# Performance work log

Measured on AMD Instinct MI355X. Metric: run time of the kernel, lower is better.

The kernel has to match this reference:

```python
import jax, jax.numpy as jnp
import numpy as np

B, LQ, LKV = 2, 4096, 2048
DQ = DK = DV = 1024
H, DQK, DHV = 16, 64, 64
DOUT = 1024


def _band_mask(span, stride):
    # additive mask: 0 where 0 <= row - col*stride < span, else -inf
    rows = jnp.arange(LQ)[:, None]
    cols = jnp.arange(LKV)[None, :]
    s = rows - cols * stride
    valid = (s >= 0) & (s < span)
    return jnp.where(valid, 0.0, -jnp.inf).astype(jnp.float32)  # [LQ, LKV]


def setup_inputs() -> dict:
    key = jax.random.key(0)
    ks = jax.random.split(key, 7)
    return {
        "q": jax.random.normal(ks[0], (B, LQ, DQ), jnp.float32),
        "k": jax.random.normal(ks[1], (B, LKV, DK), jnp.float32),
        "v": jax.random.normal(ks[2], (B, LKV, DV), jnp.float32),
        # Linear weights stored as [in, out] (x @ W == torch Linear with W.T)
        "Wq": jax.random.normal(ks[3], (DQ, H * DQK), jnp.float32) / np.sqrt(DQ).astype(np.float32),
        "Wk": jax.random.normal(ks[4], (DK, H * DQK), jnp.float32) / np.sqrt(DK).astype(np.float32),
        "Wv": jax.random.normal(ks[5], (DV, H * DHV), jnp.float32) / np.sqrt(DV).astype(np.float32),
        "Wo": jax.random.normal(ks[6], (H * DHV, DOUT), jnp.float32) / np.sqrt(H * DHV).astype(np.float32),
        "span": 16,
        "stride": 2,
    }


def reference(q, k, v, Wq, Wk, Wv, Wo, span, stride):
    mask = _band_mask(span, stride)  # [LQ, LKV]
    Q = (q @ Wq).reshape(B, LQ, H, DQK)   # [B, LQ, H, DQK]
    K = (k @ Wk).reshape(B, LKV, H, DQK)  # [B, LKV, H, DQK]
    V = (v @ Wv).reshape(B, LKV, H, DHV)  # [B, LKV, H, DHV]
    scores = jnp.einsum("bqhd,bkhd->bhqk", Q, K) + mask  # [B, H, LQ, LKV]
    # NOTE: original code softmaxes over dim 2 == the QUERY axis (faithful)
    attn = jax.nn.softmax(scores, axis=2)
    ctx = jnp.einsum("bhqk,bkhd->bqhd", attn, V).reshape(B, LQ, H * DHV)
    return ctx @ Wo  # [B, LQ, DOUT]
```

## Files before the change

### kernel.cpp

```cpp
#include <hip/hip_runtime.h>
#include <cstdint>
#include <cstddef>


typedef _Float16 f16;
typedef _Float16 f16x4 __attribute__((ext_vector_type(4)));
typedef _Float16 f16x8 __attribute__((ext_vector_type(8)));
typedef float v4f __attribute__((ext_vector_type(4)));

#define B_  2
#define LQ_ 4096
#define LKV_ 2048
#define DMODEL 1024
#define NH 16
#define HD 64
#define SPAN 16
#define STRIDE 2

#define NQ_ELEMS  ((size_t)B_ * LQ_ * DMODEL)
#define NKV_ELEMS ((size_t)B_ * LKV_ * DMODEL)

__device__ __forceinline__ void async_copy16(const f16* g, f16* l) {
    __builtin_amdgcn_global_load_lds((const __attribute__((address_space(1))) void*)g,
                                     (__attribute__((address_space(3))) void*)l, 16, 0, 0);
}

__global__ __launch_bounds__(256)
void transpose_all(const float* __restrict__ W0, const float* __restrict__ W1,
                   const float* __restrict__ W2, const float* __restrict__ W3,
                   f16* __restrict__ T0, f16* __restrict__ T1,
                   f16* __restrict__ T2, f16* __restrict__ T3) {
    const int t = threadIdx.x;
    const int bid = blockIdx.x;
    const int z = bid >> 8, rem = bid & 255;
    const int bx = rem & 15, byy = rem >> 4;
    const float* W;
    f16* Wt;
    switch (z) {
        case 0: W = W0; Wt = T0; break;
        case 1: W = W1; Wt = T1; break;
        case 2: W = W2; Wt = T2; break;
        default: W = W3; Wt = T3; break;
    }
    __shared__ float tile[64][65];
    const int r0 = byy * 64, c0 = bx * 64;
    const int tx = t & 63, ty = t >> 6;
    for (int i = ty; i < 64; i += 4)
        tile[i][tx] = W[(long)(r0 + i) * DMODEL + c0 + tx];
    __syncthreads();
    for (int i = ty; i < 64; i += 4)
        Wt[(long)(c0 + i) * DMODEL + r0 + tx] = (f16)tile[tx][i];
}

template <bool OUT_F32, bool A_F32>
__device__ __forceinline__ void gemm_body(const void* __restrict__ Av,
                                          const f16* __restrict__ Bt,
                                          void* __restrict__ Cv,
                                          int rowTile, int colTile) {
    constexpr int K = DMODEL, N = DMODEL;
    __shared__ f16 As[128 * 64];
    __shared__ f16 Bs[128 * 64];
    const int t = threadIdx.x;
    const int lane = t & 63;
    const int w = t >> 6;
    const int wm = w >> 1, wn = w & 1;
    const long rowBase = (long)rowTile * 128;
    const long colBase = (long)colTile * 128;
    const int qrow = lane & 15;
    const int quad = lane >> 4;

    v4f acc[4][4] = {};

    const int srow = t >> 3;
    const int schunk = t & 7;
    const int gchunk = schunk ^ (srow & 7);
    const f16* aptrH = (const f16*)Av + (rowBase + srow) * (long)K + gchunk * 8;
    const float* aptrF = (const float*)Av + (rowBase + srow) * (long)K + gchunk * 8;
    const f16* bptr = Bt + (colBase + srow) * (long)K + gchunk * 8;
    f16* lA = &As[srow * 64 + schunk * 8];
    f16* lB = &Bs[srow * 64 + schunk * 8];

    for (int k0 = 0; k0 < K; k0 += 64) {
#pragma unroll
        for (int i = 0; i < 4; ++i)
            async_copy16(bptr + k0 + i * 32 * (long)K, lB + i * 2048);
        if (A_F32) {
            float4 lo[4], hi[4];
#pragma unroll
            for (int i = 0; i < 4; ++i) {
                lo[i] = *(const float4*)(aptrF + k0 + i * 32 * (long)K);
                hi[i] = *(const float4*)(aptrF + k0 + i * 32 * (long)K + 4);
            }
#pragma unroll
            for (int i = 0; i < 4; ++i) {
                f16x8 o = {(f16)lo[i].x, (f16)lo[i].y, (f16)lo[i].z, (f16)lo[i].w,
                           (f16)hi[i].x, (f16)hi[i].y, (f16)hi[i].z, (f16)hi[i].w};
                *(f16x8*)(lA + i * 2048) = o;
            }
        } else {
#pragma unroll
            for (int i = 0; i < 4; ++i)
                async_copy16(aptrH + k0 + i * 32 * (long)K, lA + i * 2048);
        }
        __syncthreads();
#pragma unroll
        for (int s = 0; s < 2; ++s) {
            const int xk = (s * 4 + quad) ^ (qrow & 7);
            f16x8 af[4], bf[4];
#pragma unroll
            for (int mt = 0; mt < 4; ++mt)
                af[mt] = *(const f16x8*)(&As[(wm * 64 + mt * 16 + qrow) * 64 + xk * 8]);
#pragma unroll
            for (int nt = 0; nt < 4; ++nt)
                bf[nt] = *(const f16x8*)(&Bs[(wn * 64 + nt * 16 + qrow) * 64 + xk * 8]);
#pragma unroll
            for (int mt = 0; mt < 4; ++mt)
#pragma unroll
                for (int nt = 0; nt < 4; ++nt)
                    acc[mt][nt] = __builtin_amdgcn_mfma_f32_16x16x32_f16(
                        af[mt], bf[nt], acc[mt][nt], 0, 0, 0);
        }
        __syncthreads();
    }

#pragma unroll
    for (int mt = 0; mt < 4; ++mt)
#pragma unroll
        for (int nt = 0; nt < 4; ++nt) {
            const long col = colBase + wn * 64 + nt * 16 + qrow;
#pragma unroll
            for (int r = 0; r < 4; ++r) {
                const long row = rowBase + wm * 64 + mt * 16 + quad * 4 + r;
                if (OUT_F32)
                    ((float*)Cv)[row * (long)N + col] = acc[mt][nt][r];
                else
                    ((f16*)Cv)[row * (long)N + col] = (f16)acc[mt][nt][r];
            }
        }
}

__global__ __launch_bounds__(256, 2)
void gemm_qkv(const float* __restrict__ A0, const float* __restrict__ A1,
              const float* __restrict__ A2, const f16* __restrict__ B0,
              const f16* __restrict__ B1, const f16* __restrict__ B2,
              f16* __restrict__ C0, f16* __restrict__ C1, f16* __restrict__ C2) {
    const int id = blockIdx.x;
    const int xcd = id & 7;
    const int g = id >> 3;
    const int ct = g & 7;
    int rowIdx = (g >> 3) + xcd * 16;
    const float* A;
    const f16* Bt;
    f16* C;
    if (rowIdx < 64) {
        A = A0; Bt = B0; C = C0;
    } else if (rowIdx < 96) {
        A = A1; Bt = B1; C = C1; rowIdx -= 64;
    } else {
        A = A2; Bt = B2; C = C2; rowIdx -= 96;
    }
    gemm_body<false, true>((const void*)A, Bt, (void*)C, rowIdx, ct);
}

__global__ __launch_bounds__(256, 2)
void gemm_out(const f16* __restrict__ A, const f16* __restrict__ Bt,
              float* __restrict__ C) {
    const int id = blockIdx.x;
    const int xcd = id & 7;
    const int g = id >> 3;
    const int ct = g & 7;
    const int rowIdx = (g >> 3) + xcd * 8;
    gemm_body<true, false>((const void*)A, Bt, (void*)C, rowIdx, ct);
}

__global__ __launch_bounds__(256)
void attn_scores(const f16* __restrict__ Q, const f16* __restrict__ Km,
                 float* __restrict__ attnw) {
    const int c0 = blockIdx.x * 4, b = blockIdx.y;
    const int t = threadIdx.x;
    __shared__ f16 Qs[24 * 1032];
    __shared__ f16 Ks[4 * 1032];

#pragma unroll
    for (int it = 0; it < 12; ++it) {
        const int ch = t + 256 * it;
        const int row = ch >> 7, off = (ch & 127) * 8;
        int qq = 2 * c0 + row;
        if (qq > LQ_ - 1) qq = LQ_ - 1;
        f16x8 x = *(const f16x8*)(Q + (size_t)(b * LQ_ + qq) * DMODEL + off);
        const int h = off >> 6, bb = (off >> 3) & 7;
        *(f16x8*)(&Qs[row * 1032 + h * 64 + ((bb + h) & 7) * 8]) = x;
    }
#pragma unroll
    for (int it = 0; it < 2; ++it) {
        const int ch = t + 256 * it;
        const int row = ch >> 7, off = (ch & 127) * 8;
        f16x8 x = *(const f16x8*)(Km + (size_t)(b * LKV_ + c0 + row) * DMODEL + off);
        const int h = off >> 6, bb = (off >> 3) & 7;
        *(f16x8*)(&Ks[row * 1032 + h * 64 + ((bb + h) & 7) * 8]) = x;
    }
    __syncthreads();

    const int h = t >> 4, j = t & 15;
#pragma unroll
    for (int ci = 0; ci < 4; ++ci) {
        const int c = c0 + ci;
        const int q = STRIDE * c + j;
        const int row = 2 * ci + j;
        float a = 0.f;
#pragma unroll
        for (int bb = 0; bb < 8; ++bb) {
            const int off = h * 64 + ((bb + h) & 7) * 8;
            f16x8 qv = *(const f16x8*)(&Qs[row * 1032 + off]);
            f16x8 kv = *(const f16x8*)(&Ks[ci * 1032 + off]);
#pragma unroll
            for (int u = 0; u < 8; ++u) a += (float)qv[u] * (float)kv[u];
        }
        float s = (q < LQ_) ? a : -1e30f;
        float m = s;
#pragma unroll
        for (int o = 1; o < 16; o <<= 1) m = fmaxf(m, __shfl_xor(m, o, 64));
        float p = (q < LQ_) ? __expf(s - m) : 0.f;
        float sum = p;
#pragma unroll
        for (int o = 1; o < 16; o <<= 1) sum += __shfl_xor(sum, o, 64);
        attnw[(size_t)((b * LKV_ + c) * NH + h) * SPAN + j] = p / sum;
    }
}

__global__ __launch_bounds__(256)
void ctx_gather(const float* __restrict__ attnw, const f16* __restrict__ V,
                f16* __restrict__ ctx) {
    const int q0 = blockIdx.x * 16, b = blockIdx.y;
    const int t = threadIdx.x;
    const int kbase = (q0 >> 1) - 7;
    __shared__ f16 Vs[16 * 1024];
    __shared__ float A_lds[16 * 256];

#pragma unroll
    for (int it = 0; it < 8; ++it) {
        const int ch = t + 256 * it;
        const int row = ch >> 7, off = (ch & 127) * 8;
        int k = kbase + row;
        k = (k < 0) ? 0 : ((k > LKV_ - 1) ? LKV_ - 1 : k);
        *(f16x8*)(&Vs[row * 1024 + off]) =
            *(const f16x8*)(V + (size_t)(b * LKV_ + k) * DMODEL + off);
    }
#pragma unroll
    for (int it = 0; it < 4; ++it) {
        const int ch = t + 256 * it;
        const int row = ch >> 6, off = (ch & 63) * 4;
        int k = kbase + row;
        k = (k < 0) ? 0 : ((k > LKV_ - 1) ? LKV_ - 1 : k);
        *(float4*)(&A_lds[row * 256 + off]) =
            *(const float4*)(attnw + (size_t)(b * LKV_ + k) * 256 + off);
    }
    __syncthreads();

    const int d = t & 63;
    const int hg = t >> 6;
#pragma unroll
    for (int ql = 0; ql < 16; ++ql) {
        const int q = q0 + ql;
        const int j0 = q & 1;
        float acc[4] = {0.f, 0.f, 0.f, 0.f};
#pragma unroll
        for (int i = 0; i < SPAN / STRIDE; ++i) {
            const int kq = (q >> 1) - i;
            if (kq < 0) break;
            const int rr = kq - kbase;
#pragma unroll
            for (int hh = 0; hh < 4; ++hh) {
                const int h = hg * 4 + hh;
                acc[hh] += A_lds[rr * 256 + h * 16 + j0 + 2 * i] *
                           (float)Vs[rr * 1024 + h * 64 + d];
            }
        }
        f16* crow = ctx + (size_t)(b * LQ_ + q) * DMODEL;
#pragma unroll
        for (int hh = 0; hh < 4; ++hh) {
            const int h = hg * 4 + hh;
            crow[h * HD + d] = (f16)acc[hh];
        }
    }
}

extern "C" void kernel_launch(void* const* d_in, const int* in_sizes, int n_in,
                              void* d_out, int out_size, void* d_ws, size_t ws_size,
                              hipStream_t stream) {
    const float* q  = (const float*)d_in[0];
    const float* k  = (const float*)d_in[1];
    const float* v  = (const float*)d_in[2];
    const float* Wq = (const float*)d_in[3];
    const float* Wk = (const float*)d_in[4];
    const float* Wv = (const float*)d_in[5];
    const float* Wo = (const float*)d_in[6];
    float* out = (float*)d_out;

    const size_t NW = (size_t)DMODEL * DMODEL;

    char* p = (char*)d_ws;
    f16* WqT = (f16*)p; p += NW * 2;
    f16* WkT = (f16*)p; p += NW * 2;
    f16* WvT = (f16*)p; p += NW * 2;
    f16* WoT = (f16*)p; p += NW * 2;
    f16* Qh  = (f16*)p; p += NQ_ELEMS * 2;
    f16* Kh  = (f16*)p; p += NKV_ELEMS * 2;
    f16* Vh  = (f16*)p; p += NKV_ELEMS * 2;
    float* attnw = (float*)p; p += (size_t)B_ * LKV_ * NH * SPAN * 4;
    f16* ctxh = (f16*)p; p += NQ_ELEMS * 2;

    transpose_all<<<dim3(1024), 256, 0, stream>>>(Wq, Wk, Wv, Wo,
                                                  WqT, WkT, WvT, WoT);

    gemm_qkv<<<dim3(1024), 256, 0, stream>>>(q, k, v, WqT, WkT, WvT, Qh, Kh, Vh);

    attn_scores<<<dim3(LKV_ / 4, B_), 256, 0, stream>>>(Qh, Kh, attnw);

    ctx_gather<<<dim3(LQ_ / 16, B_), 256, 0, stream>>>(attnw, Vh, ctxh);

    gemm_out<<<dim3(512), 256, 0, stream>>>(ctxh, WoT, out);
}
```

Before: 228.0 us.

## Rewrite projection GEMMs with larger tiles and register-staged double-buffered LDS pipeline

Replaces the 128x128 single-buffered GEMM with a templated 256-row tile kernel using 512 threads. Global loads are prefetched two stages ahead into registers and written into double-buffered LDS, so only one barrier is needed per k-step. The QKV GEMM now uses 256x256 tiles and the output GEMM 256x128, with remapped XCD block ordering and s_setprio around the MFMA bursts. The aim is more data reuse per tile and better overlap of memory latency with MFMA work, at the cost of higher register and LDS pressure and fewer blocks (256 per GEMM) to fill the CUs.

```diff
diff --git a/kernel.cpp b/kernel.cpp
--- a/kernel.cpp
+++ b/kernel.cpp
@@ -4,7 +4,6 @@
 
 
 typedef _Float16 f16;
-typedef _Float16 f16x4 __attribute__((ext_vector_type(4)));
 typedef _Float16 f16x8 __attribute__((ext_vector_type(8)));
 typedef float v4f __attribute__((ext_vector_type(4)));
 
@@ -19,11 +18,6 @@
 
 #define NQ_ELEMS  ((size_t)B_ * LQ_ * DMODEL)
 #define NKV_ELEMS ((size_t)B_ * LKV_ * DMODEL)
-
-__device__ __forceinline__ void async_copy16(const f16* g, f16* l) {
-    __builtin_amdgcn_global_load_lds((const __attribute__((address_space(1))) void*)g,
-                                     (__attribute__((address_space(3))) void*)l, 16, 0, 0);
-}
 
 __global__ __launch_bounds__(256)
 void transpose_all(const float* __restrict__ W0, const float* __restrict__ W1,
@@ -52,125 +46,164 @@
         Wt[(long)(c0 + i) * DMODEL + r0 + tx] = (f16)tile[tx][i];
 }
 
-template <bool OUT_F32, bool A_F32>
-__device__ __forceinline__ void gemm_body(const void* __restrict__ Av,
+template <bool A_F32, bool OUT_F32, int BN, int WM, int WN, int MR, int NR>
+__device__ __forceinline__ void gemm_pipe(const void* __restrict__ Av,
                                           const f16* __restrict__ Bt,
                                           void* __restrict__ Cv,
                                           int rowTile, int colTile) {
-    constexpr int K = DMODEL, N = DMODEL;
-    __shared__ f16 As[128 * 64];
-    __shared__ f16 Bs[128 * 64];
+    constexpr int BM = 256, BK = 64, K = DMODEL, N = DMODEL, NT = K / BK;
+    static_assert(WM * MR * 16 == BM, "BM decomposition");
+    static_assert(WN * NR * 16 == BN, "BN decomposition");
+    constexpr int LA = BM * BK;
+    constexpr int LB = BN * BK;
+    constexpr int LT = LA + LB;
+    __shared__ f16 lds[2 * LT];
+
     const int t = threadIdx.x;
-    const int lane = t & 63;
-    const int w = t >> 6;
-    const int wm = w >> 1, wn = w & 1;
-    const long rowBase = (long)rowTile * 128;
-    const long colBase = (long)colTile * 128;
-    const int qrow = lane & 15;
-    const int quad = lane >> 4;
-
-    v4f acc[4][4] = {};
-
-    const int srow = t >> 3;
-    const int schunk = t & 7;
-    const int gchunk = schunk ^ (srow & 7);
-    const f16* aptrH = (const f16*)Av + (rowBase + srow) * (long)K + gchunk * 8;
-    const float* aptrF = (const float*)Av + (rowBase + srow) * (long)K + gchunk * 8;
-    const f16* bptr = Bt + (colBase + srow) * (long)K + gchunk * 8;
-    f16* lA = &As[srow * 64 + schunk * 8];
-    f16* lB = &Bs[srow * 64 + schunk * 8];
-
-    for (int k0 = 0; k0 < K; k0 += 64) {
-#pragma unroll
-        for (int i = 0; i < 4; ++i)
-            async_copy16(bptr + k0 + i * 32 * (long)K, lB + i * 2048);
-        if (A_F32) {
-            float4 lo[4], hi[4];
-#pragma unroll
-            for (int i = 0; i < 4; ++i) {
-                lo[i] = *(const float4*)(aptrF + k0 + i * 32 * (long)K);
-                hi[i] = *(const float4*)(aptrF + k0 + i * 32 * (long)K + 4);
-            }
-#pragma unroll
-            for (int i = 0; i < 4; ++i) {
-                f16x8 o = {(f16)lo[i].x, (f16)lo[i].y, (f16)lo[i].z, (f16)lo[i].w,
-                           (f16)hi[i].x, (f16)hi[i].y, (f16)hi[i].z, (f16)hi[i].w};
-                *(f16x8*)(lA + i * 2048) = o;
+    const int lane = t & 63, w = t >> 6;
+    const int wm = w / WN, wn = w % WN;
+    const int qrow = lane & 15, quad = lane >> 4;
+    const long rowBase = (long)rowTile * BM;
+    const long colBase = (long)colTile * BN;
+
+    const int arow = t >> 1, ah = t & 1;
+    constexpr int TPRB = 512 / BN;
+    constexpr int CPTB = 8 / TPRB;
+    const int brow = t / TPRB, bsub = t % TPRB;
+
+    const float* gAf = (const float*)Av + (rowBase + arow) * (long)K + ah * 32;
+    const f16*   gAh = (const f16*)Av + (rowBase + arow) * (long)K + ah * 32;
+    const f16*   gB  = Bt + (colBase + brow) * (long)K + bsub * (CPTB * 8);
+
+    int offA[4], offB[CPTB];
+#pragma unroll
+    for (int j = 0; j < 4; ++j)
+        offA[j] = arow * BK + (((ah * 4 + j) ^ (arow & 7)) * 8);
+#pragma unroll
+    for (int j = 0; j < CPTB; ++j)
+        offB[j] = LA + brow * BK + (((bsub * CPTB + j) ^ (brow & 7)) * 8);
+
+    int offAf[MR], offBf[NR];
+#pragma unroll
+    for (int m = 0; m < MR; ++m) offAf[m] = (wm * (MR * 16) + m * 16 + qrow) * BK;
+#pragma unroll
+    for (int n = 0; n < NR; ++n) offBf[n] = LA + (wn * (NR * 16) + n * 16 + qrow) * BK;
+
+    float4 ra[2][8];
+    f16x8  rah[2][4];
+    f16x8  rb[2][CPTB];
+    v4f acc[MR][NR] = {};
+
+    auto LOAD = [&](int tt, int ss) {
+        if constexpr (A_F32) {
+#pragma unroll
+            for (int j = 0; j < 8; ++j)
+                ra[ss][j] = *(const float4*)(gAf + tt * BK + 4 * j);
+        } else {
+#pragma unroll
+            for (int j = 0; j < 4; ++j)
+                rah[ss][j] = *(const f16x8*)(gAh + tt * BK + 8 * j);
+        }
+#pragma unroll
+        for (int j = 0; j < CPTB; ++j)
+            rb[ss][j] = *(const f16x8*)(gB + tt * BK + 8 * j);
+    };
+
+    auto WRITE = [&](int tt, int ss) {
+        f16* lp = &lds[(tt & 1) * LT];
+        if constexpr (A_F32) {
+#pragma unroll
+            for (int j = 0; j < 4; ++j) {
+                float4 lo = ra[ss][2 * j], hi = ra[ss][2 * j + 1];
+                f16x8 o = {(f16)lo.x, (f16)lo.y, (f16)lo.z, (f16)lo.w,
+                           (f16)hi.x, (f16)hi.y, (f16)hi.z, (f16)hi.w};
+                *(f16x8*)(lp + offA[j]) = o;
             }
         } else {
 #pragma unroll
-            for (int i = 0; i < 4; ++i)
-                async_copy16(aptrH + k0 + i * 32 * (long)K, lA + i * 2048);
-        }
-        __syncthreads();
+            for (int j = 0; j < 4; ++j)
+                *(f16x8*)(lp + offA[j]) = rah[ss][j];
+        }
+#pragma unroll
+        for (int j = 0; j < CPTB; ++j)
+            *(f16x8*)(lp + offB[j]) = rb[ss][j];
+    };
+
+    auto COMPUTE = [&](int tt) {
+        const f16* lp = &lds[(tt & 1) * LT];
 #pragma unroll
         for (int s = 0; s < 2; ++s) {
-            const int xk = (s * 4 + quad) ^ (qrow & 7);
-            f16x8 af[4], bf[4];
-#pragma unroll
-            for (int mt = 0; mt < 4; ++mt)
-                af[mt] = *(const f16x8*)(&As[(wm * 64 + mt * 16 + qrow) * 64 + xk * 8]);
-#pragma unroll
-            for (int nt = 0; nt < 4; ++nt)
-                bf[nt] = *(const f16x8*)(&Bs[(wn * 64 + nt * 16 + qrow) * 64 + xk * 8]);
-#pragma unroll
-            for (int mt = 0; mt < 4; ++mt)
-#pragma unroll
-                for (int nt = 0; nt < 4; ++nt)
-                    acc[mt][nt] = __builtin_amdgcn_mfma_f32_16x16x32_f16(
-                        af[mt], bf[nt], acc[mt][nt], 0, 0, 0);
-        }
-        __syncthreads();
-    }
-
-#pragma unroll
-    for (int mt = 0; mt < 4; ++mt)
-#pragma unroll
-        for (int nt = 0; nt < 4; ++nt) {
-            const long col = colBase + wn * 64 + nt * 16 + qrow;
+            const int xk = ((s * 4 + quad) ^ (qrow & 7)) * 8;
+            f16x8 afr[MR], bfr[NR];
+#pragma unroll
+            for (int m = 0; m < MR; ++m) afr[m] = *(const f16x8*)(lp + offAf[m] + xk);
+#pragma unroll
+            for (int n = 0; n < NR; ++n) bfr[n] = *(const f16x8*)(lp + offBf[n] + xk);
+            __builtin_amdgcn_s_setprio(1);
+#pragma unroll
+            for (int m = 0; m < MR; ++m)
+#pragma unroll
+                for (int n = 0; n < NR; ++n)
+                    acc[m][n] = __builtin_amdgcn_mfma_f32_16x16x32_f16(
+                        afr[m], bfr[n], acc[m][n], 0, 0, 0);
+            __builtin_amdgcn_s_setprio(0);
+        }
+    };
+
+    LOAD(0, 0);
+    LOAD(1, 1);
+    WRITE(0, 0);
+    asm volatile("s_waitcnt lgkmcnt(0)" ::: "memory");
+    __builtin_amdgcn_s_barrier();
+    asm volatile("" ::: "memory");
+
+#pragma unroll
+    for (int tt = 0; tt < NT; ++tt) {
+        if (tt + 1 < NT) WRITE(tt + 1, (tt + 1) & 1);
+        if (tt + 2 < NT) LOAD(tt + 2, tt & 1);
+        COMPUTE(tt);
+        if (tt + 1 < NT) {
+            asm volatile("s_waitcnt lgkmcnt(0)" ::: "memory");
+            __builtin_amdgcn_s_barrier();
+            asm volatile("" ::: "memory");
+        }
+    }
+
+#pragma unroll
+    for (int m = 0; m < MR; ++m)
+#pragma unroll
+        for (int n = 0; n < NR; ++n) {
+            const long col = colBase + wn * (NR * 16) + n * 16 + qrow;
 #pragma unroll
             for (int r = 0; r < 4; ++r) {
-                const long row = rowBase + wm * 64 + mt * 16 + quad * 4 + r;
-                if (OUT_F32)
-                    ((float*)Cv)[row * (long)N + col] = acc[mt][nt][r];
+                const long row = rowBase + wm * (MR * 16) + m * 16 + quad * 4 + r;
+                if constexpr (OUT_F32)
+                    ((float*)Cv)[row * (long)N + col] = acc[m][n][r];
                 else
-                    ((f16*)Cv)[row * (long)N + col] = (f16)acc[mt][nt][r];
+                    ((f16*)Cv)[row * (long)N + col] = (f16)acc[m][n][r];
             }
         }
 }
 
-__global__ __launch_bounds__(256, 2)
-void gemm_qkv(const float* __restrict__ A0, const float* __restrict__ A1,
-              const float* __restrict__ A2, const f16* __restrict__ B0,
-              const f16* __restrict__ B1, const f16* __restrict__ B2,
-              f16* __restrict__ C0, f16* __restrict__ C1, f16* __restrict__ C2) {
-    const int id = blockIdx.x;
-    const int xcd = id & 7;
-    const int g = id >> 3;
-    const int ct = g & 7;
-    int rowIdx = (g >> 3) + xcd * 16;
-    const float* A;
-    const f16* Bt;
-    f16* C;
-    if (rowIdx < 64) {
-        A = A0; Bt = B0; C = C0;
-    } else if (rowIdx < 96) {
-        A = A1; Bt = B1; C = C1; rowIdx -= 64;
-    } else {
-        A = A2; Bt = B2; C = C2; rowIdx -= 96;
-    }
-    gemm_body<false, true>((const void*)A, Bt, (void*)C, rowIdx, ct);
-}
-
-__global__ __launch_bounds__(256, 2)
+__global__ __launch_bounds__(512, 2)
+void gemm_qkv(const float* __restrict__ q, const float* __restrict__ k,
+              const float* __restrict__ v, const f16* __restrict__ WqT,
+              const f16* __restrict__ WkT, const f16* __restrict__ WvT,
+              f16* __restrict__ Qh, f16* __restrict__ Kh, f16* __restrict__ Vh) {
+    const int id = (blockIdx.x & 7) * 32 + (blockIdx.x >> 3);
+    const float* A; const f16* Bt; f16* C; int rt, ct;
+    if (id < 128)      { A = q; Bt = WqT; C = Qh; ct = id >> 5; rt = id & 31; }
+    else if (id < 192) { const int g = id - 128; A = k; Bt = WkT; C = Kh; ct = g >> 4; rt = g & 15; }
+    else               { const int g = id - 192; A = v; Bt = WvT; C = Vh; ct = g >> 4; rt = g & 15; }
+    gemm_pipe<true, false, 256, 2, 4, 8, 4>((const void*)A, Bt, (void*)C, rt, ct);
+}
+
+__global__ __launch_bounds__(512, 2)
 void gemm_out(const f16* __restrict__ A, const f16* __restrict__ Bt,
               float* __restrict__ C) {
-    const int id = blockIdx.x;
-    const int xcd = id & 7;
-    const int g = id >> 3;
-    const int ct = g & 7;
-    const int rowIdx = (g >> 3) + xcd * 8;
-    gemm_body<true, false>((const void*)A, Bt, (void*)C, rowIdx, ct);
+    const int id = (blockIdx.x & 7) * 32 + (blockIdx.x >> 3);
+    const int ct = id >> 5, rt = id & 31;
+    gemm_pipe<false, true, 128, 4, 2, 4, 4>((const void*)A, Bt, (void*)C, rt, ct);
 }
 
 __global__ __launch_bounds__(256)
@@ -313,11 +346,11 @@
     transpose_all<<<dim3(1024), 256, 0, stream>>>(Wq, Wk, Wv, Wo,
                                                   WqT, WkT, WvT, WoT);
 
-    gemm_qkv<<<dim3(1024), 256, 0, stream>>>(q, k, v, WqT, WkT, WvT, Qh, Kh, Vh);
+    gemm_qkv<<<dim3(256), 512, 0, stream>>>(q, k, v, WqT, WkT, WvT, Qh, Kh, Vh);
 
     attn_scores<<<dim3(LKV_ / 4, B_), 256, 0, stream>>>(Qh, Kh, attnw);
 
     ctx_gather<<<dim3(LQ_ / 16, B_), 256, 0, stream>>>(attnw, Vh, ctxh);
 
-    gemm_out<<<dim3(512), 256, 0, stream>>>(ctxh, WoT, out);
-}
+    gemm_out<<<dim3(256), 512, 0, stream>>>(ctxh, WoT, out);
+}
```

After: 248.2 us. 8.9% more time.
